# Performance work log

Measured on AMD Instinct MI355X. Metric: run time of the kernel, lower is better.

Reference implementation:

```python
import jax, jax.numpy as jnp
import numpy as np

B, HF, WF, C, A = 8, 32, 32, 1024, 9
N = B * HF * WF * A
IMG = 1024.0
K = 512                 # fixed candidate cap (replaces dynamic tf.where shape)
NUM_CLASSES = 80
FRCNN_FEAT = 256
ALIGN, SAMPLES = 7, 2
DET_THR, NMS_IOU = 0.7, 0.7
BN_EPS = 1e-3


def setup_inputs() -> dict:
    key = jax.random.key(0)
    ks = jax.random.split(key, 8)
    rpn_predictions = jax.random.normal(ks[0], (N,), jnp.float32)

    def rand_boxes(k):
        k1, k2, k3, k4 = jax.random.split(k, 4)
        cy = jax.random.uniform(k1, (N,), minval=0.0, maxval=IMG)
        cx = jax.random.uniform(k2, (N,), minval=0.0, maxval=IMG)
        h = jax.random.uniform(k3, (N,), minval=32.0, maxval=256.0)
        w = jax.random.uniform(k4, (N,), minval=32.0, maxval=256.0)
        return cy, cx, h, w

    cy, cx, h, w = rand_boxes(ks[1])
    rpn_anchors = jnp.stack([cy, cx, h, w], -1)  # center-point format [y,x,h,w]
    cy2, cx2, h2, w2 = rand_boxes(ks[2])
    rpn_rois = jnp.stack([
        jnp.clip(cy2 - h2 / 2, 0, IMG), jnp.clip(cx2 - w2 / 2, 0, IMG),
        jnp.clip(cy2 + h2 / 2, 0, IMG), jnp.clip(cx2 + w2 / 2, 0, IMG)], -1)
    rpn_assignments = jnp.repeat(jnp.arange(B, dtype=jnp.int32), HF * WF * A)
    images_features = jax.random.normal(ks[3], (B, HF, WF, C), jnp.float32)
    W1 = jax.random.normal(ks[4], (C, FRCNN_FEAT), jnp.float32) * 0.02
    b1 = jnp.zeros((FRCNN_FEAT,), jnp.float32)
    gamma = jnp.ones((FRCNN_FEAT,), jnp.float32)
    beta = jnp.zeros((FRCNN_FEAT,), jnp.float32)
    moving_mean = jnp.zeros((FRCNN_FEAT,), jnp.float32)
    moving_var = jnp.ones((FRCNN_FEAT,), jnp.float32)
    W2 = jax.random.normal(ks[5], (FRCNN_FEAT, 4 + NUM_CLASSES), jnp.float32) * 0.02
    b2 = jnp.zeros((4 + NUM_CLASSES,), jnp.float32)
    return dict(rpn_predictions=rpn_predictions, rpn_rois=rpn_rois,
                rpn_anchors=rpn_anchors, rpn_assignments=rpn_assignments,
                images_features=images_features, W1=W1, b1=b1, gamma=gamma,
                beta=beta, moving_mean=moving_mean, moving_var=moving_var,
                W2=W2, b2=b2)


def center_to_corners(a):
    y, x, h, w = a[:, 0], a[:, 1], a[:, 2], a[:, 3]
    return jnp.stack([y - h / 2, x - w / 2, y + h / 2, x + w / 2], -1)


def iou_one(box, boxes):
    yA = jnp.maximum(box[0], boxes[:, 0]); xA = jnp.maximum(box[1], boxes[:, 1])
    yB = jnp.minimum(box[2], boxes[:, 2]); xB = jnp.minimum(box[3], boxes[:, 3])
    inter = jnp.maximum(yB - yA, 0.0) * jnp.maximum(xB - xA, 0.0)
    a1 = (box[2] - box[0]) * (box[3] - box[1])
    a2 = (boxes[:, 2] - boxes[:, 0]) * (boxes[:, 3] - boxes[:, 1])
    return inter / (a1 + a2 - inter + 1e-8)


def greedy_nms(boxes, valid, thr):
    # boxes are already in score-descending order
    k = boxes.shape[0]
    idxs = jnp.arange(k)
    def body(i, keep):
        sup = (iou_one(boxes[i], boxes) > thr) & (idxs > i) & keep[i]
        return keep & ~sup
    return jax.lax.fori_loop(0, k, body, valid)


def roi_align_mean(feats, rois_n, assign):
    # feats [B,H,W,C]; rois_n [K,4] normalized corners; assign [K] batch idx
    Bf, H, W, Cf = feats.shape
    Kc = rois_n.shape[0]
    y1 = rois_n[:, 0] * H; x1 = rois_n[:, 1] * W
    y2 = rois_n[:, 2] * H; x2 = rois_n[:, 3] * W
    S = ALIGN * SAMPLES  # 14 samples per axis
    frac = (jnp.arange(S, dtype=feats.dtype) + 0.5) / S
    ys = y1[:, None] + frac * (y2 - y1)[:, None] - 0.5  # [K,S]
    xs = x1[:, None] + frac * (x2 - x1)[:, None] - 0.5
    yy = jnp.broadcast_to(ys[:, :, None], (Kc, S, S)).reshape(Kc, S * S)
    xx = jnp.broadcast_to(xs[:, None, :], (Kc, S, S)).reshape(Kc, S * S)
    yc = jnp.clip(yy, 0.0, H - 1.0); xc = jnp.clip(xx, 0.0, W - 1.0)
    y0 = jnp.floor(yc); x0 = jnp.floor(xc)
    wy = yc - y0; wx = xc - x0
    y0i = y0.astype(jnp.int32); x0i = x0.astype(jnp.int32)
    y1i = jnp.minimum(y0i + 1, H - 1); x1i = jnp.minimum(x0i + 1, W - 1)
    flat = feats.reshape(Bf * H * W, Cf)
    base = (assign.astype(jnp.int32) * H * W)[:, None]
    def g(yi, xi):
        return flat[(base + yi * W + xi).reshape(-1)].reshape(Kc, S * S, Cf)
    val = (((1 - wy) * (1 - wx))[..., None] * g(y0i, x0i)
           + ((1 - wy) * wx)[..., None] * g(y0i, x1i)
           + (wy * (1 - wx))[..., None] * g(y1i, x0i)
           + (wy * wx)[..., None] * g(y1i, x1i))
    # mean over all samples == mean over the 7x7 bins of per-bin sample means
    return val.mean(axis=1)  # [K,C]


def reference(rpn_predictions, rpn_rois, rpn_anchors, rpn_assignments,
              images_features, W1, b1, gamma, beta, moving_mean, moving_var,
              W2, b2):
    boxes_norm = jnp.array([IMG, IMG, IMG, IMG], jnp.float32)
    # --- threshold + gather (fixed-K top-k replaces dynamic tf.where) ---
    masked = jnp.where(rpn_predictions > DET_THR, rpn_predictions, -jnp.inf)
    top_scores, idx = jax.lax.top_k(masked, K)
    valid = jnp.isfinite(top_scores)
    rois = rpn_rois[idx]
    anchors = rpn_anchors[idx]
    assign = rpn_assignments[idx]
    # --- shift anchors per-image so NMS runs jointly across the batch ---
    shifted = center_to_corners(anchors) + assign[:, None].astype(jnp.float32) * boxes_norm
    # sigmoid is monotone -> score-descending order already holds
    keep = greedy_nms(shifted, valid, NMS_IOU)
    # --- ROI align + head (computed on all K, masked by keep) ---
    pooled = roi_align_mean(images_features, rois / boxes_norm, assign)  # [K,C]
    hdd = pooled @ W1 + b1
    hdd = (hdd - moving_mean) * jax.lax.rsqrt(moving_var + BN_EPS) * gamma + beta
    hdd = jax.nn.relu(hdd)  # dropout inactive at inference
    out = hdd @ W2 + b2  # [K, 4+num_classes]
    keepf = keep.astype(out.dtype)[:, None]
    frcnn_rois = (rois + out[:, :4]) * keepf
    frcnn_predictions = out[:, 4:] * keepf
    return frcnn_predictions, frcnn_rois, keep
```

## Files before the change

### kernel.cpp

```cpp
#include <hip/hip_runtime.h>
#include <stdint.h>

#define NTOT   73728
#define KSEL   512
#define DET_THRf 0.7f
#define NMS_THRf 0.7f
#define HFD    32
#define WFD    32
#define CCH    1024
#define IMGF   1024.0f
#define SAMP   14
#define FEAT1  256
#define OUTD   84
#define MAXC   4096
#define BUCKETS 256
#define BSCALE 48.0f

#define WS_HIST     0
#define WS_CUTB     1024
#define WS_COUNTER  1028
#define WS_CSCORE   1040
#define WS_CIDX     17424
#define WS_SELIDX   33824
#define WS_VALID    35872
#define WS_ASSIGN   37920
#define WS_ROIS     39968
#define WS_BOXES    48160
#define WS_KEEPF    56352
#define WS_SUP      58400

__device__ __forceinline__ int bucket_of(float s) {
  int b = (int)((s - DET_THRf) * BSCALE);
  return min(max(b, 0), BUCKETS - 1);
}

__global__ void k_hist(const float* __restrict__ pred, int* __restrict__ hist) {
  __shared__ int lh[BUCKETS];
  int t = threadIdx.x;
  lh[t] = 0;
  __syncthreads();
  for (int i = blockIdx.x * blockDim.x + t; i < NTOT; i += gridDim.x * blockDim.x) {
    float s = pred[i];
    if (s > DET_THRf) atomicAdd(&lh[bucket_of(s)], 1);
  }
  __syncthreads();
  if (lh[t]) atomicAdd(&hist[t], lh[t]);
}

__global__ void k_scan(const int* __restrict__ hist, int* __restrict__ cutB) {
  if (threadIdx.x == 0) {
    int cum = 0, B = 0;
    for (int b = BUCKETS - 1; b >= 0; --b) {
      cum += hist[b];
      if (cum >= KSEL) { B = b; break; }
    }
    *cutB = B;
  }
}

__global__ void k_collect(const float* __restrict__ pred, const int* __restrict__ cutB,
                          int* __restrict__ counter, float* __restrict__ cs,
                          int* __restrict__ ci) {
  int B = *cutB;
  for (int i = blockIdx.x * blockDim.x + threadIdx.x; i < NTOT; i += gridDim.x * blockDim.x) {
    float s = pred[i];
    if (s > DET_THRf && bucket_of(s) >= B) {
      int p = atomicAdd(counter, 1);
      if (p < MAXC) { cs[p] = s; ci[p] = i; }
    }
  }
}

__global__ void __launch_bounds__(512) k_select(
    const int* __restrict__ counter, const float* __restrict__ cs, const int* __restrict__ ci,
    const float* __restrict__ rois, const float* __restrict__ anchors,
    const int* __restrict__ assign,
    int* __restrict__ sel_idx, int* __restrict__ valid, int* __restrict__ assign_sel,
    float4* __restrict__ rois_sel, float4* __restrict__ boxes_sh) {
  __shared__ float s_s[MAXC];
  __shared__ int   s_i[MAXC];
  int t = threadIdx.x;
  int M = *counter; if (M > MAXC) M = MAXC;
  for (int j = t; j < M; j += 512) { s_s[j] = cs[j]; s_i[j] = ci[j]; }
  if (t < KSEL) { sel_idx[t] = 0; valid[t] = 0; }
  __syncthreads();
  for (int j = t; j < M; j += 512) {
    float sj = s_s[j]; int ij = s_i[j];
    int r = 0;
    for (int m = 0; m < M; ++m) {
      float sm = s_s[m];
      r += (sm > sj) || (sm == sj && s_i[m] < ij);
    }
    if (r < KSEL) { sel_idx[r] = ij; valid[r] = 1; }
  }
  __syncthreads();
  if (t < KSEL) {
    int v = valid[t];
    int gi = v ? sel_idx[t] : 0;
    float4 rr = make_float4(0.f, 0.f, 0.f, 0.f);
    float4 bx = make_float4(0.f, 0.f, 0.f, 0.f);
    int aa = 0;
    if (v) {
      rr = make_float4(rois[gi*4+0], rois[gi*4+1], rois[gi*4+2], rois[gi*4+3]);
      float cy = anchors[gi*4+0], cx = anchors[gi*4+1];
      float h  = anchors[gi*4+2], w  = anchors[gi*4+3];
      aa = assign[gi];
      float off = (float)aa * IMGF;
      bx = make_float4(cy - h*0.5f + off, cx - w*0.5f + off,
                       cy + h*0.5f + off, cx + w*0.5f + off);
    }
    rois_sel[t] = rr;
    boxes_sh[t] = bx;
    assign_sel[t] = aa;
  }
}

__global__ void k_ioumat(const float4* __restrict__ boxes,
                         unsigned long long* __restrict__ sup) {
  int wave = (blockIdx.x * blockDim.x + threadIdx.x) >> 6;
  int lane = threadIdx.x & 63;
  if (wave >= KSEL) return;
  float4 bi = boxes[wave];
  float a1 = (bi.z - bi.x) * (bi.w - bi.y);
  for (int c = 0; c < 8; ++c) {
    int col = c * 64 + lane;
    float4 bj = boxes[col];
    float yA = fmaxf(bi.x, bj.x), xA = fmaxf(bi.y, bj.y);
    float yB = fminf(bi.z, bj.z), xB = fminf(bi.w, bj.w);
    float inter = fmaxf(yB - yA, 0.f) * fmaxf(xB - xA, 0.f);
    float a2 = (bj.z - bj.x) * (bj.w - bj.y);
    float iou = inter / (a1 + a2 - inter + 1e-8f);
    bool s = (iou > NMS_THRf) && (col > wave);
    unsigned long long m = __ballot(s);
    if (lane == 0) sup[wave * 8 + c] = m;
  }
}

__global__ void k_sweep(const unsigned long long* __restrict__ sup,
                        const int* __restrict__ valid,
                        float* __restrict__ keep_ws, float* __restrict__ keep_out) {
  __shared__ unsigned char kb[KSEL];
  int t = threadIdx.x;
  for (int j = t; j < KSEL; j += 64) kb[j] = (unsigned char)valid[j];
  unsigned long long nz[8];
  for (int w = 0; w < 8; ++w) {
    int row = w * 64 + t;
    const unsigned long long* rp = &sup[row * 8];
    unsigned long long any = rp[0]|rp[1]|rp[2]|rp[3]|rp[4]|rp[5]|rp[6]|rp[7];
    nz[w] = __ballot(any != 0ull);
  }
  __syncthreads();
  if (t == 0) {
    for (int w = 0; w < 8; ++w) {
      unsigned long long bits = nz[w];
      while (bits) {
        int b = __ffsll((unsigned long long)bits) - 1;
        bits &= bits - 1;
        int i = w * 64 + b;
        if (kb[i]) {
          const unsigned long long* rp = &sup[i * 8];
          for (int c = 0; c < 8; ++c) {
            unsigned long long m = rp[c];
            while (m) {
              int bb = __ffsll((unsigned long long)m) - 1;
              m &= m - 1;
              kb[c * 64 + bb] = 0;
            }
          }
        }
      }
    }
  }
  __syncthreads();
  for (int j = t; j < KSEL; j += 64) {
    float kf = kb[j] ? 1.0f : 0.0f;
    keep_ws[j] = kf;
    keep_out[j] = kf;
  }
}

__global__ void __launch_bounds__(256) k_head(
    const float* __restrict__ feats,
    const float* __restrict__ W1, const float* __restrict__ b1,
    const float* __restrict__ gamma, const float* __restrict__ beta,
    const float* __restrict__ mmean, const float* __restrict__ mvar,
    const float* __restrict__ W2, const float* __restrict__ b2,
    const float4* __restrict__ rois_sel, const int* __restrict__ assign_sel,
    const float* __restrict__ keepf_ws,
    float* __restrict__ pred_out, float* __restrict__ rois_out) {
  int r = blockIdx.x;
  int t = threadIdx.x;

  float kf = keepf_ws[r];
  float4 roi = rois_sel[r];
  if (kf == 0.0f) {
    for (int j = t; j < 80; j += 256) pred_out[r * 80 + j] = 0.f;
    if (t < 4) rois_out[r * 4 + t] = 0.f;
    return;
  }

  __shared__ float Wy[HFD], Wx[WFD];
  __shared__ int bnds[4];
  __shared__ float pooled[CCH];
  __shared__ float hdd[FEAT1];
  __shared__ float outv[OUTD];

  if (t < 32) { Wy[t] = 0.f; Wx[t] = 0.f; }
  __syncthreads();
  if (t == 0) {
    float sc = (float)HFD / IMGF;
    float y1 = roi.x * sc, x1 = roi.y * sc, y2 = roi.z * sc, x2 = roi.w * sc;
    int ymin = HFD - 1, ymax = 0, xmin = WFD - 1, xmax = 0;
    for (int s = 0; s < SAMP; ++s) {
      float fr = ((float)s + 0.5f) / (float)SAMP;
      float yc = y1 + fr * (y2 - y1) - 0.5f;
      yc = fminf(fmaxf(yc, 0.0f), (float)(HFD - 1));
      float y0f = floorf(yc);
      int y0 = (int)y0f;
      int y1i = min(y0 + 1, HFD - 1);
      float wy = yc - y0f;
      Wy[y0] += 1.0f - wy;
      Wy[y1i] += wy;
      ymin = min(ymin, y0); ymax = max(ymax, y1i);

      float xc = x1 + fr * (x2 - x1) - 0.5f;
      xc = fminf(fmaxf(xc, 0.0f), (float)(WFD - 1));
      float x0f = floorf(xc);
      int x0 = (int)x0f;
      int x1i = min(x0 + 1, WFD - 1);
      float wx = xc - x0f;
      Wx[x0] += 1.0f - wx;
      Wx[x1i] += wx;
      xmin = min(xmin, x0); xmax = max(xmax, x1i);
    }
    bnds[0] = ymin; bnds[1] = ymax; bnds[2] = xmin; bnds[3] = xmax;
  }
  __syncthreads();

  int b = assign_sel[r];
  const float4* f4 = (const float4*)feats;
  float4 acc = make_float4(0.f, 0.f, 0.f, 0.f);
  int ymin = bnds[0], ymax = bnds[1], xmin = bnds[2], xmax = bnds[3];
  for (int y = ymin; y <= ymax; ++y) {
    float wyv = Wy[y];
    int rowbase = ((b * HFD + y) * WFD) * (CCH / 4);
    for (int x = xmin; x <= xmax; ++x) {
      float w = wyv * Wx[x];
      float4 v = f4[rowbase + x * (CCH / 4) + t];
      acc.x += w * v.x; acc.y += w * v.y; acc.z += w * v.z; acc.w += w * v.w;
    }
  }
  const float inv = 1.0f / (float)(SAMP * SAMP);
  pooled[4 * t + 0] = acc.x * inv;
  pooled[4 * t + 1] = acc.y * inv;
  pooled[4 * t + 2] = acc.z * inv;
  pooled[4 * t + 3] = acc.w * inv;
  __syncthreads();

  float h = b1[t];
  #pragma unroll 8
  for (int c = 0; c < CCH; ++c) h += pooled[c] * W1[c * FEAT1 + t];
  h = (h - mmean[t]) * rsqrtf(mvar[t] + 1e-3f) * gamma[t] + beta[t];
  hdd[t] = fmaxf(h, 0.f);
  __syncthreads();

  if (t < OUTD) {
    float o = b2[t];
    #pragma unroll 8
    for (int k = 0; k < FEAT1; ++k) o += hdd[k] * W2[k * OUTD + t];
    outv[t] = o;
  }
  __syncthreads();

  for (int j = t; j < 80; j += 256) pred_out[r * 80 + j] = outv[4 + j] * kf;
  if (t < 4) {
    float rc = (t == 0) ? roi.x : (t == 1) ? roi.y : (t == 2) ? roi.z : roi.w;
    rois_out[r * 4 + t] = (rc + outv[t]) * kf;
  }
}

extern "C" void kernel_launch(void* const* d_in, const int* in_sizes, int n_in,
                              void* d_out, int out_size, void* d_ws, size_t ws_size,
                              hipStream_t stream) {
  const float* pred    = (const float*)d_in[0];
  const float* rois    = (const float*)d_in[1];
  const float* anchors = (const float*)d_in[2];
  const int*   assign  = (const int*)d_in[3];
  const float* feats   = (const float*)d_in[4];
  const float* W1      = (const float*)d_in[5];
  const float* b1      = (const float*)d_in[6];
  const float* gamma   = (const float*)d_in[7];
  const float* beta    = (const float*)d_in[8];
  const float* mmean   = (const float*)d_in[9];
  const float* mvar    = (const float*)d_in[10];
  const float* W2      = (const float*)d_in[11];
  const float* b2      = (const float*)d_in[12];

  char* ws = (char*)d_ws;
  int*   hist     = (int*)(ws + WS_HIST);
  int*   cutB     = (int*)(ws + WS_CUTB);
  int*   counter  = (int*)(ws + WS_COUNTER);
  float* cscore   = (float*)(ws + WS_CSCORE);
  int*   cidx     = (int*)(ws + WS_CIDX);
  int*   sel_idx  = (int*)(ws + WS_SELIDX);
  int*   validp   = (int*)(ws + WS_VALID);
  int*   asel     = (int*)(ws + WS_ASSIGN);
  float4* rois_sel = (float4*)(ws + WS_ROIS);
  float4* boxes_sh = (float4*)(ws + WS_BOXES);
  float* keepf    = (float*)(ws + WS_KEEPF);
  unsigned long long* sup = (unsigned long long*)(ws + WS_SUP);

  float* pred_out = (float*)d_out;
  float* rois_out = pred_out + KSEL * 80;
  float* keep_out = rois_out + KSEL * 4;

  hipMemsetAsync(ws, 0, 1040, stream);

  k_hist<<<64, BUCKETS, 0, stream>>>(pred, hist);
  k_scan<<<1, 64, 0, stream>>>(hist, cutB);
  k_collect<<<64, 256, 0, stream>>>(pred, cutB, counter, cscore, cidx);
  k_select<<<1, 512, 0, stream>>>(counter, cscore, cidx, rois, anchors, assign,
                                  sel_idx, validp, asel, rois_sel, boxes_sh);
  k_ioumat<<<128, 256, 0, stream>>>(boxes_sh, sup);
  k_sweep<<<1, 64, 0, stream>>>(sup, validp, keepf, keep_out);
  k_head<<<KSEL, 256, 0, stream>>>(feats, W1, b1, gamma, beta, mmean, mvar,
                                   W2, b2, rois_sel, asel, keepf,
                                   pred_out, rois_out);
}
```

Baseline: 213.1 us.

## Parallelize rank selection, split head into pooling and batched FC kernels

```diff
diff --git a/kernel.cpp b/kernel.cpp
--- a/kernel.cpp
+++ b/kernel.cpp
@@ -15,19 +15,21 @@
 #define MAXC   4096
 #define BUCKETS 256
 #define BSCALE 48.0f
+#define RB     4
 
 #define WS_HIST     0
 #define WS_CUTB     1024
 #define WS_COUNTER  1028
-#define WS_CSCORE   1040
-#define WS_CIDX     17424
-#define WS_SELIDX   33824
-#define WS_VALID    35872
-#define WS_ASSIGN   37920
-#define WS_ROIS     39968
-#define WS_BOXES    48160
-#define WS_KEEPF    56352
-#define WS_SUP      58400
+#define WS_VALID    1032
+#define WS_SELIDX   3080
+#define WS_CSCORE   5136
+#define WS_CIDX     21520
+#define WS_ROIS     37904
+#define WS_BOXES    46096
+#define WS_ASSIGN   54288
+#define WS_KEEPF    56336
+#define WS_SUP      58384
+#define WS_POOLED   91152
 
 __device__ __forceinline__ int bucket_of(float s) {
   int b = (int)((s - DET_THRf) * BSCALE);
@@ -48,14 +50,21 @@
 }
 
 __global__ void k_scan(const int* __restrict__ hist, int* __restrict__ cutB) {
-  if (threadIdx.x == 0) {
-    int cum = 0, B = 0;
-    for (int b = BUCKETS - 1; b >= 0; --b) {
-      cum += hist[b];
-      if (cum >= KSEL) { B = b; break; }
-    }
-    *cutB = B;
-  }
+  __shared__ int sh[BUCKETS];
+  __shared__ int best;
+  int t = threadIdx.x;
+  sh[t] = hist[t];
+  if (t == 0) best = -1;
+  __syncthreads();
+  for (int off = 1; off < BUCKETS; off <<= 1) {
+    int v = sh[t] + ((t + off < BUCKETS) ? sh[t + off] : 0);
+    __syncthreads();
+    sh[t] = v;
+    __syncthreads();
+  }
+  if (sh[t] >= KSEL) atomicMax(&best, t);
+  __syncthreads();
+  if (t == 0) *cutB = (best < 0) ? 0 : best;
 }
 
 __global__ void k_collect(const float* __restrict__ pred, const int* __restrict__ cutB,
@@ -71,48 +80,50 @@
   }
 }
 
-__global__ void __launch_bounds__(512) k_select(
+__global__ void __launch_bounds__(256) k_rank(
     const int* __restrict__ counter, const float* __restrict__ cs, const int* __restrict__ ci,
-    const float* __restrict__ rois, const float* __restrict__ anchors,
-    const int* __restrict__ assign,
-    int* __restrict__ sel_idx, int* __restrict__ valid, int* __restrict__ assign_sel,
-    float4* __restrict__ rois_sel, float4* __restrict__ boxes_sh) {
+    int* __restrict__ sel_idx, int* __restrict__ valid) {
   __shared__ float s_s[MAXC];
   __shared__ int   s_i[MAXC];
   int t = threadIdx.x;
   int M = *counter; if (M > MAXC) M = MAXC;
-  for (int j = t; j < M; j += 512) { s_s[j] = cs[j]; s_i[j] = ci[j]; }
-  if (t < KSEL) { sel_idx[t] = 0; valid[t] = 0; }
-  __syncthreads();
-  for (int j = t; j < M; j += 512) {
-    float sj = s_s[j]; int ij = s_i[j];
-    int r = 0;
-    for (int m = 0; m < M; ++m) {
-      float sm = s_s[m];
-      r += (sm > sj) || (sm == sj && s_i[m] < ij);
-    }
-    if (r < KSEL) { sel_idx[r] = ij; valid[r] = 1; }
-  }
-  __syncthreads();
-  if (t < KSEL) {
-    int v = valid[t];
-    int gi = v ? sel_idx[t] : 0;
-    float4 rr = make_float4(0.f, 0.f, 0.f, 0.f);
-    float4 bx = make_float4(0.f, 0.f, 0.f, 0.f);
-    int aa = 0;
-    if (v) {
-      rr = make_float4(rois[gi*4+0], rois[gi*4+1], rois[gi*4+2], rois[gi*4+3]);
-      float cy = anchors[gi*4+0], cx = anchors[gi*4+1];
-      float h  = anchors[gi*4+2], w  = anchors[gi*4+3];
-      aa = assign[gi];
-      float off = (float)aa * IMGF;
-      bx = make_float4(cy - h*0.5f + off, cx - w*0.5f + off,
-                       cy + h*0.5f + off, cx + w*0.5f + off);
-    }
-    rois_sel[t] = rr;
-    boxes_sh[t] = bx;
-    assign_sel[t] = aa;
-  }
+  for (int j = t; j < M; j += 256) { s_s[j] = cs[j]; s_i[j] = ci[j]; }
+  __syncthreads();
+  int j = blockIdx.x * 256 + t;
+  if (j >= M) return;
+  float sj = s_s[j]; int ij = s_i[j];
+  int r = 0;
+  for (int m = 0; m < M; ++m) {
+    float sm = s_s[m];
+    r += (sm > sj) || (sm == sj && s_i[m] < ij);
+  }
+  if (r < KSEL) { sel_idx[r] = ij; valid[r] = 1; }
+}
+
+__global__ void k_gather(const int* __restrict__ sel_idx, const int* __restrict__ valid,
+                         const float* __restrict__ rois, const float* __restrict__ anchors,
+                         const int* __restrict__ assign,
+                         int* __restrict__ assign_sel, float4* __restrict__ rois_sel,
+                         float4* __restrict__ boxes_sh) {
+  int t = threadIdx.x;
+  if (t >= KSEL) return;
+  int v = valid[t];
+  int gi = v ? sel_idx[t] : 0;
+  float4 rr = make_float4(0.f, 0.f, 0.f, 0.f);
+  float4 bx = make_float4(0.f, 0.f, 0.f, 0.f);
+  int aa = 0;
+  if (v) {
+    rr = make_float4(rois[gi*4+0], rois[gi*4+1], rois[gi*4+2], rois[gi*4+3]);
+    float cy = anchors[gi*4+0], cx = anchors[gi*4+1];
+    float h  = anchors[gi*4+2], w  = anchors[gi*4+3];
+    aa = assign[gi];
+    float off = (float)aa * IMGF;
+    bx = make_float4(cy - h*0.5f + off, cx - w*0.5f + off,
+                     cy + h*0.5f + off, cx + w*0.5f + off);
+  }
+  rois_sel[t] = rr;
+  boxes_sh[t] = bx;
+  assign_sel[t] = aa;
 }
 
 __global__ void k_ioumat(const float4* __restrict__ boxes,
@@ -179,35 +190,22 @@
   }
 }
 
-__global__ void __launch_bounds__(256) k_head(
+__global__ void __launch_bounds__(256) k_pool(
     const float* __restrict__ feats,
-    const float* __restrict__ W1, const float* __restrict__ b1,
-    const float* __restrict__ gamma, const float* __restrict__ beta,
-    const float* __restrict__ mmean, const float* __restrict__ mvar,
-    const float* __restrict__ W2, const float* __restrict__ b2,
     const float4* __restrict__ rois_sel, const int* __restrict__ assign_sel,
-    const float* __restrict__ keepf_ws,
-    float* __restrict__ pred_out, float* __restrict__ rois_out) {
+    float* __restrict__ pooled) {
   int r = blockIdx.x;
   int t = threadIdx.x;
-
-  float kf = keepf_ws[r];
-  float4 roi = rois_sel[r];
-  if (kf == 0.0f) {
-    for (int j = t; j < 80; j += 256) pred_out[r * 80 + j] = 0.f;
-    if (t < 4) rois_out[r * 4 + t] = 0.f;
-    return;
-  }
 
   __shared__ float Wy[HFD], Wx[WFD];
   __shared__ int bnds[4];
-  __shared__ float pooled[CCH];
-  __shared__ float hdd[FEAT1];
-  __shared__ float outv[OUTD];
+  __shared__ float wcomb[128];
+  __shared__ int   ocomb[128];
 
   if (t < 32) { Wy[t] = 0.f; Wx[t] = 0.f; }
   __syncthreads();
   if (t == 0) {
+    float4 roi = rois_sel[r];
     float sc = (float)HFD / IMGF;
     float y1 = roi.x * sc, x1 = roi.y * sc, y2 = roi.z * sc, x2 = roi.w * sc;
     int ymin = HFD - 1, ymax = 0, xmin = WFD - 1, xmax = 0;
@@ -237,45 +235,109 @@
   }
   __syncthreads();
 
+  int ymin = bnds[0], xmin = bnds[2];
+  int spanY = bnds[1] - ymin + 1;
+  int spanX = bnds[3] - xmin + 1;
+  int np = spanY * spanX;
   int b = assign_sel[r];
+  const float inv = 1.0f / (float)(SAMP * SAMP);
+
+  int ty = t >> 4, tx = t & 15;
+  if (ty < spanY && tx < spanX) {
+    int p = ty * spanX + tx;
+    int y = ymin + ty, x = xmin + tx;
+    wcomb[p] = Wy[y] * Wx[x] * inv;
+    ocomb[p] = ((b * HFD + y) * WFD + x) * (CCH / 4);
+  }
+  __syncthreads();
+
   const float4* f4 = (const float4*)feats;
-  float4 acc = make_float4(0.f, 0.f, 0.f, 0.f);
-  int ymin = bnds[0], ymax = bnds[1], xmin = bnds[2], xmax = bnds[3];
-  for (int y = ymin; y <= ymax; ++y) {
-    float wyv = Wy[y];
-    int rowbase = ((b * HFD + y) * WFD) * (CCH / 4);
-    for (int x = xmin; x <= xmax; ++x) {
-      float w = wyv * Wx[x];
-      float4 v = f4[rowbase + x * (CCH / 4) + t];
-      acc.x += w * v.x; acc.y += w * v.y; acc.z += w * v.z; acc.w += w * v.w;
-    }
-  }
-  const float inv = 1.0f / (float)(SAMP * SAMP);
-  pooled[4 * t + 0] = acc.x * inv;
-  pooled[4 * t + 1] = acc.y * inv;
-  pooled[4 * t + 2] = acc.z * inv;
-  pooled[4 * t + 3] = acc.w * inv;
-  __syncthreads();
-
-  float h = b1[t];
-  #pragma unroll 8
-  for (int c = 0; c < CCH; ++c) h += pooled[c] * W1[c * FEAT1 + t];
-  h = (h - mmean[t]) * rsqrtf(mvar[t] + 1e-3f) * gamma[t] + beta[t];
-  hdd[t] = fmaxf(h, 0.f);
-  __syncthreads();
-
-  if (t < OUTD) {
-    float o = b2[t];
-    #pragma unroll 8
-    for (int k = 0; k < FEAT1; ++k) o += hdd[k] * W2[k * OUTD + t];
-    outv[t] = o;
-  }
-  __syncthreads();
-
-  for (int j = t; j < 80; j += 256) pred_out[r * 80 + j] = outv[4 + j] * kf;
-  if (t < 4) {
-    float rc = (t == 0) ? roi.x : (t == 1) ? roi.y : (t == 2) ? roi.z : roi.w;
-    rois_out[r * 4 + t] = (rc + outv[t]) * kf;
+  float4 a0 = make_float4(0.f,0.f,0.f,0.f), a1 = a0, a2 = a0, a3 = a0;
+  int p = 0;
+  for (; p + 4 <= np; p += 4) {
+    float w0 = wcomb[p],   w1 = wcomb[p+1], w2 = wcomb[p+2], w3 = wcomb[p+3];
+    int   o0 = ocomb[p],   o1 = ocomb[p+1], o2 = ocomb[p+2], o3 = ocomb[p+3];
+    float4 v0 = f4[o0 + t], v1 = f4[o1 + t], v2 = f4[o2 + t], v3 = f4[o3 + t];
+    a0.x += w0*v0.x; a0.y += w0*v0.y; a0.z += w0*v0.z; a0.w += w0*v0.w;
+    a1.x += w1*v1.x; a1.y += w1*v1.y; a1.z += w1*v1.z; a1.w += w1*v1.w;
+    a2.x += w2*v2.x; a2.y += w2*v2.y; a2.z += w2*v2.z; a2.w += w2*v2.w;
+    a3.x += w3*v3.x; a3.y += w3*v3.y; a3.z += w3*v3.z; a3.w += w3*v3.w;
+  }
+  for (; p < np; ++p) {
+    float w = wcomb[p];
+    float4 v = f4[ocomb[p] + t];
+    a0.x += w*v.x; a0.y += w*v.y; a0.z += w*v.z; a0.w += w*v.w;
+  }
+  float4 s;
+  s.x = (a0.x + a1.x) + (a2.x + a3.x);
+  s.y = (a0.y + a1.y) + (a2.y + a3.y);
+  s.z = (a0.z + a1.z) + (a2.z + a3.z);
+  s.w = (a0.w + a1.w) + (a2.w + a3.w);
+  ((float4*)pooled)[r * (CCH / 4) + t] = s;
+}
+
+__global__ void __launch_bounds__(256) k_fc(
+    const float* __restrict__ pooled,
+    const float* __restrict__ W1, const float* __restrict__ b1,
+    const float* __restrict__ gamma, const float* __restrict__ beta,
+    const float* __restrict__ mmean, const float* __restrict__ mvar,
+    const float* __restrict__ W2, const float* __restrict__ b2,
+    const float4* __restrict__ rois_sel, const float* __restrict__ keepf,
+    float* __restrict__ pred_out, float* __restrict__ rois_out) {
+  int r0 = blockIdx.x * RB;
+  int t = threadIdx.x;
+  __shared__ float hdd[RB][FEAT1];
+  __shared__ float outv[RB][OUTD];
+
+  const float* p0 = pooled + (r0 + 0) * CCH;
+  const float* p1 = pooled + (r0 + 1) * CCH;
+  const float* p2 = pooled + (r0 + 2) * CCH;
+  const float* p3 = pooled + (r0 + 3) * CCH;
+
+  float acc0 = 0.f, acc1 = 0.f, acc2 = 0.f, acc3 = 0.f;
+  for (int c = 0; c < CCH; c += 4) {
+    #pragma unroll
+    for (int u = 0; u < 4; ++u) {
+      float w = W1[(c + u) * FEAT1 + t];
+      acc0 += p0[c + u] * w;
+      acc1 += p1[c + u] * w;
+      acc2 += p2[c + u] * w;
+      acc3 += p3[c + u] * w;
+    }
+  }
+  float bb = b1[t];
+  float mn = mmean[t];
+  float iv = rsqrtf(mvar[t] + 1e-3f) * gamma[t];
+  float bt = beta[t];
+  hdd[0][t] = fmaxf((acc0 + bb - mn) * iv + bt, 0.f);
+  hdd[1][t] = fmaxf((acc1 + bb - mn) * iv + bt, 0.f);
+  hdd[2][t] = fmaxf((acc2 + bb - mn) * iv + bt, 0.f);
+  hdd[3][t] = fmaxf((acc3 + bb - mn) * iv + bt, 0.f);
+  __syncthreads();
+
+  for (int idx = t; idx < RB * OUTD; idx += 256) {
+    int r = idx / OUTD, o = idx - OUTD * r;
+    float s = b2[o];
+    for (int k = 0; k < FEAT1; k += 4) {
+      float4 h4 = *(const float4*)&hdd[r][k];
+      s += h4.x * W2[(k+0) * OUTD + o];
+      s += h4.y * W2[(k+1) * OUTD + o];
+      s += h4.z * W2[(k+2) * OUTD + o];
+      s += h4.w * W2[(k+3) * OUTD + o];
+    }
+    outv[r][o] = s;
+  }
+  __syncthreads();
+
+  for (int idx = t; idx < RB * 80; idx += 256) {
+    int r = idx / 80, j = idx - 80 * r;
+    pred_out[(r0 + r) * 80 + j] = outv[r][4 + j] * keepf[r0 + r];
+  }
+  if (t < RB * 4) {
+    int r = t >> 2, c = t & 3;
+    float4 roi = rois_sel[r0 + r];
+    float rc = (c == 0) ? roi.x : (c == 1) ? roi.y : (c == 2) ? roi.z : roi.w;
+    rois_out[(r0 + r) * 4 + c] = (rc + outv[r][c]) * keepf[r0 + r];
   }
 }
 
@@ -300,30 +362,33 @@
   int*   hist     = (int*)(ws + WS_HIST);
   int*   cutB     = (int*)(ws + WS_CUTB);
   int*   counter  = (int*)(ws + WS_COUNTER);
+  int*   validp   = (int*)(ws + WS_VALID);
+  int*   sel_idx  = (int*)(ws + WS_SELIDX);
   float* cscore   = (float*)(ws + WS_CSCORE);
   int*   cidx     = (int*)(ws + WS_CIDX);
-  int*   sel_idx  = (int*)(ws + WS_SELIDX);
-  int*   validp   = (int*)(ws + WS_VALID);
-  int*   asel     = (int*)(ws + WS_ASSIGN);
   float4* rois_sel = (float4*)(ws + WS_ROIS);
   float4* boxes_sh = (float4*)(ws + WS_BOXES);
+  int*   asel     = (int*)(ws + WS_ASSIGN);
   float* keepf    = (float*)(ws + WS_KEEPF);
   unsigned long long* sup = (unsigned long long*)(ws + WS_SUP);
+  float* pooled   = (float*)(ws + WS_POOLED);
 
   float* pred_out = (float*)d_out;
   float* rois_out = pred_out + KSEL * 80;
   float* keep_out = rois_out + KSEL * 4;
 
-  hipMemsetAsync(ws, 0, 1040, stream);
+  hipMemsetAsync(ws, 0, 3080, stream);
 
   k_hist<<<64, BUCKETS, 0, stream>>>(pred, hist);
-  k_scan<<<1, 64, 0, stream>>>(hist, cutB);
+  k_scan<<<1, BUCKETS, 0, stream>>>(hist, cutB);
   k_collect<<<64, 256, 0, stream>>>(pred, cutB, counter, cscore, cidx);
-  k_select<<<1, 512, 0, stream>>>(counter, cscore, cidx, rois, anchors, assign,
-                                  sel_idx, validp, asel, rois_sel, boxes_sh);
+  k_rank<<<MAXC / 256, 256, 0, stream>>>(counter, cscore, cidx, sel_idx, validp);
+  k_gather<<<1, KSEL, 0, stream>>>(sel_idx, validp, rois, anchors, assign,
+                                   asel, rois_sel, boxes_sh);
   k_ioumat<<<128, 256, 0, stream>>>(boxes_sh, sup);
   k_sweep<<<1, 64, 0, stream>>>(sup, validp, keepf, keep_out);
-  k_head<<<KSEL, 256, 0, stream>>>(feats, W1, b1, gamma, beta, mmean, mvar,
-                                   W2, b2, rois_sel, asel, keepf,
-                                   pred_out, rois_out);
-}
+  k_pool<<<KSEL, 256, 0, stream>>>(feats, rois_sel, asel, pooled);
+  k_fc<<<KSEL / RB, 256, 0, stream>>>(pooled, W1, b1, gamma, beta, mmean, mvar,
+                                      W2, b2, rois_sel, keepf,
+                                      pred_out, rois_out);
+}
```

Measured after the change: 212.9 us. Within noise of the previous version (-0.1%).
